# Performance work log

Measured on AMD Instinct MI355X. Metric: run time of the kernel, lower is better.

## Reference

```python
import jax, jax.numpy as jnp
import numpy as np

B, S, D, H = 4, 1024, 1024, 16
DK = D // H
MASK_WEIGHT_0 = 1.0   # weight for key-type 0 (from (weight, mask_mat) tuple)
MASK_WEIGHT_1 = 0.5   # weight for key-type 1
NEG_INF = -1.0e9


def setup_inputs() -> dict:
    key = jax.random.key(0)
    ks = jax.random.split(key, 10)
    wscale = 0.02
    return {
        "query": jax.random.normal(ks[0], (B, S, D), jnp.float32),
        "key_x": jax.random.normal(ks[1], (B, S, D), jnp.float32),
        "value": jax.random.normal(ks[2], (B, S, D), jnp.float32),
        "mask0": jax.random.randint(ks[3], (B, S, S), 0, 2, jnp.int32),
        "mask1": jax.random.randint(ks[4], (B, S, S), 0, 2, jnp.int32),
        "Wq":  wscale * jax.random.normal(ks[5], (D, D), jnp.float32),
        "Wk0": wscale * jax.random.normal(ks[6], (D, D), jnp.float32),
        "Wk1": wscale * jax.random.normal(ks[7], (D, D), jnp.float32),
        "Wv":  wscale * jax.random.normal(ks[8], (D, D), jnp.float32),
        "Wo":  wscale * jax.random.normal(ks[9], (D, D), jnp.float32),
    }


def _heads(x, W):
    # torch nn.Linear: x @ W.T ; then view(B,S,H,DK).transpose(1,2)
    return (x @ W.T).reshape(B, S, H, DK).transpose(0, 2, 1, 3)  # [B,H,S,DK]


def reference(query, key_x, value, mask0, mask1, Wq, Wk0, Wk1, Wv, Wo):
    q = _heads(query, Wq)          # [B,H,S,DK]
    k0 = _heads(key_x, Wk0)
    k1 = _heads(key_x, Wk1)
    v = _heads(value, Wv)
    scale = 1.0 / jnp.sqrt(jnp.float32(DK))

    def masked_score(k, mask, weight):
        s = jnp.einsum('bhqd,bhkd->bhqk', q, k) * scale       # [B,H,S,S]
        keep = (mask != 0)[:, None, :, :]                     # broadcast over heads
        # (score * weight*keep).masked_fill(mask==0, -1e9)
        return jnp.where(keep, s * weight, NEG_INF)

    scores = masked_score(k0, mask0, MASK_WEIGHT_0) + masked_score(k1, mask1, MASK_WEIGHT_1)
    p_attn = jax.nn.sigmoid(scores)                           # activation='sigmoid'
    x = jnp.einsum('bhqk,bhkd->bhqd', p_attn, v)              # [B,H,S,DK]
    x = x.transpose(0, 2, 1, 3).reshape(B, S, D)
    return x @ Wo.T                                            # output_linear (dropout p=0)
```

## Files before the change

### kernel.cpp

```cpp
#include <hip/hip_runtime.h>

#define B_  4
#define S_  1024
#define D_  1024
#define H_  16
#define DK_ 64

typedef __attribute__((ext_vector_type(8)))  short bf16x8;
typedef __attribute__((ext_vector_type(4)))  short bf16x4;
typedef __attribute__((ext_vector_type(4)))  float f32x4;
typedef __attribute__((ext_vector_type(16))) float f32x16;

static __device__ __forceinline__ unsigned short f2bf(float f) {
  union { float f; unsigned u; } v; v.f = f;
  unsigned r = v.u + 0x7FFFu + ((v.u >> 16) & 1u);
  return (unsigned short)(r >> 16);
}

static __device__ __forceinline__ unsigned cvtpk(float lo, float hi) {
  unsigned r;
  asm("v_cvt_pk_bf16_f32 %0, %1, %2" : "=v"(r) : "v"(lo), "v"(hi));
  return r;
}
static __device__ __forceinline__ void plswap(unsigned &a, unsigned &b) {
  asm volatile("v_permlane32_swap_b32 %0, %1" : "+v"(a), "+v"(b));
}

typedef __attribute__((address_space(1))) const void gc_t;
typedef __attribute__((address_space(3))) void lds_t;
static __device__ __forceinline__ void gload_lds16(const void* g, void* l) {
  __builtin_amdgcn_global_load_lds((gc_t*)g, (lds_t*)l, 16, 0, 0);
}

#define TM_ (1u << 22)
#define WM_ (1u << 20)

#define CEXP_ (-0.18033688011112042f)

__global__ __launch_bounds__(256)
void prep(const float* __restrict__ q, const float* __restrict__ k,
          const float* __restrict__ v,
          const float* __restrict__ w0, const float* __restrict__ w1,
          const float* __restrict__ w2, const float* __restrict__ w3,
          const float* __restrict__ w4, unsigned short* __restrict__ out,
          const int* __restrict__ m0, const int* __restrict__ m1,
          unsigned long long* __restrict__ pk)
{
  if (blockIdx.x < 8192) {
    const size_t u = ((size_t)blockIdx.x * 256 + threadIdx.x) * 8;
    unsigned short t[8];
    unsigned short* dst;
    size_t off;
    if (u < (size_t)3 * TM_) {
      int seg = (int)(u >> 22); off = u & (TM_ - 1);
      const float* src = seg == 0 ? q : (seg == 1 ? k : v);
      dst = out + (size_t)seg * TM_ + off;
      float4 f0 = *(const float4*)(src + off);
      float4 f1 = *(const float4*)(src + off + 4);
      t[0]=f2bf(f0.x); t[1]=f2bf(f0.y); t[2]=f2bf(f0.z); t[3]=f2bf(f0.w);
      t[4]=f2bf(f1.x); t[5]=f2bf(f1.y); t[6]=f2bf(f1.z); t[7]=f2bf(f1.w);
    } else {
      size_t uu = u - (size_t)3 * TM_;
      int seg = (int)(uu >> 20); off = uu & (WM_ - 1);
      dst = out + (size_t)3 * TM_ + (size_t)seg * WM_ + off;
      if (seg == 0) {
        float4 f0 = *(const float4*)(w0 + off);
        float4 f1 = *(const float4*)(w0 + off + 4);
        t[0]=f2bf(CEXP_*f0.x); t[1]=f2bf(CEXP_*f0.y);
        t[2]=f2bf(CEXP_*f0.z); t[3]=f2bf(CEXP_*f0.w);
        t[4]=f2bf(CEXP_*f1.x); t[5]=f2bf(CEXP_*f1.y);
        t[6]=f2bf(CEXP_*f1.z); t[7]=f2bf(CEXP_*f1.w);
      } else if (seg == 1) {
        float4 a0 = *(const float4*)(w1 + off);
        float4 a1 = *(const float4*)(w1 + off + 4);
        float4 b0 = *(const float4*)(w2 + off);
        float4 b1 = *(const float4*)(w2 + off + 4);
        t[0]=f2bf(a0.x+0.5f*b0.x); t[1]=f2bf(a0.y+0.5f*b0.y);
        t[2]=f2bf(a0.z+0.5f*b0.z); t[3]=f2bf(a0.w+0.5f*b0.w);
        t[4]=f2bf(a1.x+0.5f*b1.x); t[5]=f2bf(a1.y+0.5f*b1.y);
        t[6]=f2bf(a1.z+0.5f*b1.z); t[7]=f2bf(a1.w+0.5f*b1.w);
      } else {
        const float* src = (seg == 2) ? w3 : w4;
        float4 f0 = *(const float4*)(src + off);
        float4 f1 = *(const float4*)(src + off + 4);
        t[0]=f2bf(f0.x); t[1]=f2bf(f0.y); t[2]=f2bf(f0.z); t[3]=f2bf(f0.w);
        t[4]=f2bf(f1.x); t[5]=f2bf(f1.y); t[6]=f2bf(f1.z); t[7]=f2bf(f1.w);
      }
    }
    *(bf16x8*)dst = *(bf16x8*)t;
  } else {
    const int bidm = blockIdx.x - 8192;
    const int wid  = bidm * 4 + (threadIdx.x >> 6);
    const int lane = threadIdx.x & 63;
    const int word = wid & 15, row = wid >> 4;
    const size_t g = (size_t)row * S_ + word * 64 + lane;
    const bool bit = (m0[g] != 0) & (m1[g] != 0);
    const unsigned long long m = __ballot(bit);
    if (lane == 0) pk[wid] = m;
  }
}

__global__ __launch_bounds__(256, 4)
void proj_gemm(const unsigned short* __restrict__ qbf,
               const unsigned short* __restrict__ kbf,
               const unsigned short* __restrict__ vbf,
               const unsigned short* __restrict__ wbf,
               unsigned short* __restrict__ Qb, unsigned short* __restrict__ Kh,
               unsigned short* __restrict__ Vth)
{
  __shared__ unsigned short As[128][64];
  __shared__ unsigned short Ws[128][64];

  const int tid = threadIdx.x, bid = blockIdx.x;
  const int xcd = bid & 7, c = bid >> 3;
  const int L = xcd * 96 + c;
  const int which = L >> 8;
  const int rem = L & 255;
  const int nt = rem >> 5, mt = rem & 31;
  const int m0 = mt * 128, n0 = nt * 128;
  const int w = tid >> 6, l = tid & 63;
  const int lr = l & 15, lg = l >> 4;
  const int wr = w >> 1, wc = w & 1;

  const unsigned short* A = (which == 0) ? qbf : (which == 1) ? kbf : vbf;
  const unsigned short* W = wbf + (size_t)which * WM_;

  const f32x4 fzero = {0.f, 0.f, 0.f, 0.f};
  f32x4 acc[4][4];
#pragma unroll
  for (int m = 0; m < 4; m++)
#pragma unroll
    for (int n = 0; n < 4; n++) acc[m][n] = fzero;

  const int srow8 = l >> 3;
  const int sg    = ((l & 7) ^ srow8) * 8;
  const int rc0 = ((lg)     ^ (lr & 7)) * 8;
  const int rc1 = ((4 + lg) ^ (lr & 7)) * 8;

  const unsigned short* aBase = A + (size_t)(m0 + w*32 + srow8) * 1024 + sg;
  const unsigned short* wBase = W + (size_t)(n0 + w*32 + srow8) * 1024 + sg;

  for (int kk = 0; kk < 1024; kk += 64) {
#pragma unroll
    for (int cc = 0; cc < 4; ++cc)
      gload_lds16(aBase + (size_t)cc * 8 * 1024 + kk, &As[w*32 + cc*8][0]);
#pragma unroll
    for (int cc = 0; cc < 4; ++cc)
      gload_lds16(wBase + (size_t)cc * 8 * 1024 + kk, &Ws[w*32 + cc*8][0]);
    __syncthreads();

#pragma unroll
    for (int ks = 0; ks < 2; ++ks) {
      const int rc = ks ? rc1 : rc0;
      bf16x8 af[4], bfr[4];
#pragma unroll
      for (int m = 0; m < 4; m++) af[m]  = *(const bf16x8*)&As[wr*64 + m*16 + lr][rc];
#pragma unroll
      for (int n = 0; n < 4; n++) bfr[n] = *(const bf16x8*)&Ws[wc*64 + n*16 + lr][rc];
#pragma unroll
      for (int m = 0; m < 4; m++)
#pragma unroll
        for (int n = 0; n < 4; n++)
          acc[m][n] = __builtin_amdgcn_mfma_f32_16x16x32_bf16(af[m], bfr[n], acc[m][n], 0, 0, 0);
    }
    __syncthreads();
  }

  if (which == 2) {
#pragma unroll
    for (int m = 0; m < 4; m++) {
      const int row = m0 + wr*64 + m*16 + lg*4;
      const int b = row >> 10, s = row & 1023;
#pragma unroll
      for (int n = 0; n < 4; n++) {
        const int col = n0 + wc*64 + n*16 + lr;
        const int h = col >> 6, dk = col & 63;
        unsigned short tv[4] = {f2bf(acc[m][n][0]), f2bf(acc[m][n][1]),
                                f2bf(acc[m][n][2]), f2bf(acc[m][n][3])};
        const size_t a = ((size_t)((b*H_ + h)*DK_ + dk)) * S_
                       + (size_t)(s & ~63) + ((((s >> 3) & 7) ^ (dk & 7)) << 3) + (s & 7);
        *(bf16x4*)(Vth + a) = *(bf16x4*)tv;
      }
    }
  } else if (which == 0) {
#pragma unroll
    for (int m = 0; m < 4; m++) {
      const int row = m0 + wr*64 + m*16 + lg*4;
#pragma unroll
      for (int n = 0; n < 4; n++) {
        const int col = n0 + wc*64 + n*16 + lr;
#pragma unroll
        for (int r = 0; r < 4; r++)
          Qb[(size_t)(row + r) * 1024 + col] = f2bf(acc[m][n][r]);
      }
    }
  } else {
#pragma unroll
    for (int m = 0; m < 4; m++) {
      const int row = m0 + wr*64 + m*16 + lg*4;
#pragma unroll
      for (int n = 0; n < 4; n++) {
        const int col = n0 + wc*64 + n*16 + lr;
        const int h = col >> 6, dk = col & 63;
#pragma unroll
        for (int r = 0; r < 4; r++) {
          const int rr = row + r;
          const int b = rr >> 10, s = rr & 1023;
          const size_t a = ((size_t)((b*H_ + h)*S_ + s)) * 64
                         + (((dk >> 3) ^ (s & 7)) << 3) + (dk & 7);
          Kh[a] = f2bf(acc[m][n][r]);
        }
      }
    }
  }
}

__global__ __launch_bounds__(256, 4)
void out_gemm(const unsigned short* __restrict__ A,
              const unsigned short* __restrict__ W, float* __restrict__ C)
{
  __shared__ unsigned short As[128][64];
  __shared__ unsigned short Ws2[64][64];

  const int tid = threadIdx.x, bid = blockIdx.x;
  const int xcd = bid & 7, idx = bid >> 3;
  const int mt = (xcd << 2) | (idx & 3);
  const int nt = idx >> 2;
  const int m0 = mt * 128, n0 = nt * 64;
  const int w = tid >> 6, l = tid & 63;
  const int lr = l & 15, lg = l >> 4;
  const int wr = w >> 1, wc = w & 1;

  const f32x4 fzero = {0.f, 0.f, 0.f, 0.f};
  f32x4 acc[4][2];
#pragma unroll
  for (int m = 0; m < 4; m++)
#pragma unroll
    for (int n = 0; n < 2; n++) acc[m][n] = fzero;

  const int srow8 = l >> 3;
  const int sg    = ((l & 7) ^ srow8) * 8;
  const int rc0 = ((lg)     ^ (lr & 7)) * 8;
  const int rc1 = ((4 + lg) ^ (lr & 7)) * 8;

  const unsigned short* aBase = A + (size_t)(m0 + w*32 + srow8) * 1024 + sg;
  const unsigned short* wBase = W + (size_t)(n0 + w*16 + srow8) * 1024 + sg;

  for (int kk = 0; kk < 1024; kk += 64) {
#pragma unroll
    for (int cc = 0; cc < 4; ++cc)
      gload_lds16(aBase + (size_t)cc * 8 * 1024 + kk, &As[w*32 + cc*8][0]);
#pragma unroll
    for (int cc = 0; cc < 2; ++cc)
      gload_lds16(wBase + (size_t)cc * 8 * 1024 + kk, &Ws2[w*16 + cc*8][0]);
    __syncthreads();

#pragma unroll
    for (int ks = 0; ks < 2; ++ks) {
      const int rc = ks ? rc1 : rc0;
      bf16x8 af[4], bfr[2];
#pragma unroll
      for (int m = 0; m < 4; m++) af[m]  = *(const bf16x8*)&As[wr*64 + m*16 + lr][rc];
#pragma unroll
      for (int n = 0; n < 2; n++) bfr[n] = *(const bf16x8*)&Ws2[wc*32 + n*16 + lr][rc];
#pragma unroll
      for (int m = 0; m < 4; m++)
#pragma unroll
        for (int n = 0; n < 2; n++)
          acc[m][n] = __builtin_amdgcn_mfma_f32_16x16x32_bf16(af[m], bfr[n], acc[m][n], 0, 0, 0);
    }
    __syncthreads();
  }

#pragma unroll
  for (int m = 0; m < 4; m++) {
    const int row = m0 + wr*64 + m*16 + lg*4;
#pragma unroll
    for (int n = 0; n < 2; n++) {
      const int col = n0 + wc*32 + n*16 + lr;
#pragma unroll
      for (int r = 0; r < 4; r++)
        C[(size_t)(row + r) * 1024 + col] = acc[m][n][r];
    }
  }
}

__global__ __launch_bounds__(512)
void attn_kernel(const unsigned short* __restrict__ Q,
                 const unsigned short* __restrict__ Kh,
                 const unsigned short* __restrict__ Vth,
                 const unsigned long long* __restrict__ mpk,
                 unsigned short* __restrict__ X)
{
  __shared__ unsigned short Ks[2][2][4096];
  __shared__ unsigned short Vs[2][2][4096];

  const int tid  = threadIdx.x;
  const int bid0 = blockIdx.x;
  const int bid = ((bid0 & 7) << 6) | (bid0 >> 3);
  const int qt = bid & 7, h = (bid >> 3) & 15, b = bid >> 7;
  const int q0 = qt * 128;
  const int w8 = tid >> 6, lw = tid & 63;
  const int grp = w8 >> 2, qw = w8 & 3;
  const int l31 = lw & 31, hh = lw >> 5, l7 = lw & 7;
  const int bh = b * H_ + h;

  bf16x8 qf[4];
  {
    const unsigned short* qp = Q + ((size_t)(b*S_ + q0 + qw*32 + l31)) * D_ + h*DK_ + hh*8;
#pragma unroll
    for (int ds = 0; ds < 4; ++ds) qf[ds] = *(const bf16x8*)(qp + ds*16);
  }
  const size_t mbase = ((size_t)(b*S_ + q0 + qw*32 + l31)) * 16 + grp*8;

  f32x16 acc0, acc1;
#pragma unroll
  for (int r = 0; r < 16; ++r) { acc0[r] = 0.f; acc1[r] = 0.f; }

  const unsigned short* gp[4];
  unsigned short* lb[4];
  int stp[4];
#pragma unroll
  for (int c = 0; c < 4; ++c) {
    const int e = qw*4 + c;
    const int bu = e >> 3, s = e & 7;
    lb[c] = (bu == 0 ? &Ks[grp][0][0] : &Vs[grp][0][0]) + s*512;
    if (bu == 0) {
      gp[c]  = Kh + (size_t)bh * 65536 + grp*32768 + s*512 + lw*8;
      stp[c] = 4096;
    } else {
      gp[c]  = Vth + ((size_t)(bh*DK_ + s*8 + (lw >> 3))) * S_ + grp*512 + (lw & 7) * 8;
      stp[c] = 64;
    }
  }

#define STAGE(nxt)                                                     \
  {                                                                    \
    _Pragma("unroll")                                                  \
    for (int c = 0; c < 4; ++c) {                                      \
      gload_lds16(gp[c], lb[c] + (nxt)*4096);                          \
      gp[c] += stp[c];                                                 \
    }                                                                  \
  }

  STAGE(0);
  __syncthreads();
  unsigned long long mw = mpk[mbase];
  int cur = 0;

  for (int t = 0; t < 8; ++t) {
    unsigned long long mw_n = 0;
    if (t < 7) { STAGE(cur ^ 1); mw_n = mpk[mbase + t + 1]; }

#pragma unroll
    for (int sub = 0; sub < 2; ++sub) {
      const int rbase = (sub*32 + l31) * 64;
      f32x16 sv;
#pragma unroll
      for (int r = 0; r < 16; ++r) sv[r] = 0.f;
      __builtin_amdgcn_s_setprio(1);
#pragma unroll
      for (int ds = 0; ds < 4; ++ds) {
        const int g = (((ds*2 + hh) ^ l7)) * 8;
        const bf16x8 kf = *(const bf16x8*)&Ks[grp][cur][rbase + g];
        sv = __builtin_amdgcn_mfma_f32_32x32x16_bf16(kf, qf[ds], sv, 0, 0, 0);
      }
      __builtin_amdgcn_s_setprio(0);

      const unsigned am = (unsigned)(mw >> (sub*32 + 4*hh));
      float p[16];
#pragma unroll
      for (int r = 0; r < 16; ++r) {
        const int cbit = (r & 3) + 8*(r >> 2);
        const float e  = __builtin_amdgcn_exp2f(sv[r]);
        const float pr = __builtin_amdgcn_rcpf(1.0f + e);
        p[r] = ((am >> cbit) & 1u) ? pr : 0.f;
      }

      bf16x8 pa[2];
#pragma unroll
      for (int ks = 0; ks < 2; ++ks) {
        const int a0 = ks*8;
        unsigned u0 = cvtpk(p[a0+0], p[a0+1]);
        unsigned u1 = cvtpk(p[a0+2], p[a0+3]);
        unsigned u2 = cvtpk(p[a0+4], p[a0+5]);
        unsigned u3 = cvtpk(p[a0+6], p[a0+7]);
        plswap(u0, u2);
        plswap(u1, u3);
        union { unsigned u[4]; bf16x8 v; } pu;
        pu.u[0] = u0; pu.u[1] = u1; pu.u[2] = u2; pu.u[3] = u3;
        pa[ks] = pu.v;
      }

      __builtin_amdgcn_s_setprio(1);
#pragma unroll
      for (int ks = 0; ks < 2; ++ks) {
        const int g = ((sub*4 + ks*2 + hh) ^ l7) * 8;
        const bf16x8 vb0 = *(const bf16x8*)&Vs[grp][cur][(l31)      * 64 + g];
        const bf16x8 vb1 = *(const bf16x8*)&Vs[grp][cur][(32 + l31) * 64 + g];
        acc0 = __builtin_amdgcn_mfma_f32_32x32x16_bf16(pa[ks], vb0, acc0, 0, 0, 0);
        acc1 = __builtin_amdgcn_mfma_f32_32x32x16_bf16(pa[ks], vb1, acc1, 0, 0, 0);
      }
      __builtin_amdgcn_s_setprio(0);
    }

    if (t < 7) {
      __syncthreads();
      mw = mw_n;
      cur ^= 1;
    }
  }
#undef STAGE

  __syncthreads();
  float2* cmb = (float2*)&Ks[0][0][0];
  if (grp == 1) {
#pragma unroll
    for (int i = 0; i < 8; ++i)
      cmb[(qw*16 + i)*64 + lw] = make_float2(acc0[2*i], acc0[2*i+1]);
#pragma unroll
    for (int i = 0; i < 8; ++i)
      cmb[(qw*16 + 8 + i)*64 + lw] = make_float2(acc1[2*i], acc1[2*i+1]);
  }
  __syncthreads();
  if (grp == 0) {
#pragma unroll
    for (int i = 0; i < 8; ++i) {
      float2 v = cmb[(qw*16 + i)*64 + lw];
      acc0[2*i] += v.x; acc0[2*i+1] += v.y;
    }
#pragma unroll
    for (int i = 0; i < 8; ++i) {
      float2 v = cmb[(qw*16 + 8 + i)*64 + lw];
      acc1[2*i] += v.x; acc1[2*i+1] += v.y;
    }
#pragma unroll
    for (int r = 0; r < 16; ++r) {
      const int qrow = q0 + qw*32 + (r & 3) + 8*(r >> 2) + 4*hh;
      unsigned short* xp = X + ((size_t)(b*S_ + qrow)) * D_ + h*DK_ + l31;
      xp[0]  = f2bf(acc0[r]);
      xp[32] = f2bf(acc1[r]);
    }
  }
}

extern "C" void kernel_launch(void* const* d_in, const int* in_sizes, int n_in,
                              void* d_out, int out_size, void* d_ws, size_t ws_size,
                              hipStream_t stream)
{
  const float* query = (const float*)d_in[0];
  const float* key_x = (const float*)d_in[1];
  const float* value = (const float*)d_in[2];
  const int*   mask0 = (const int*)d_in[3];
  const int*   mask1 = (const int*)d_in[4];
  const float* Wq    = (const float*)d_in[5];
  const float* Wk0   = (const float*)d_in[6];
  const float* Wk1   = (const float*)d_in[7];
  const float* Wv    = (const float*)d_in[8];
  const float* Wo    = (const float*)d_in[9];

  unsigned short* ws = (unsigned short*)d_ws;
  unsigned short* qbf = ws;
  unsigned short* kbf = ws + (size_t)TM_;
  unsigned short* vbf = ws + (size_t)2 * TM_;
  unsigned short* wbf = ws + (size_t)3 * TM_;
  unsigned short* Qb  = ws + (size_t)3 * TM_ + 4 * WM_;
  unsigned short* Kh  = Qb  + (size_t)TM_;
  unsigned short* Vth = Kh  + (size_t)TM_;
  unsigned long long* mpk = (unsigned long long*)(Vth + (size_t)TM_);
  unsigned short* Xb = qbf;

  prep<<<dim3(8192 + 16384), dim3(256), 0, stream>>>(
      query, key_x, value, Wq, Wk0, Wk1, Wv, Wo, ws, mask0, mask1, mpk);

  proj_gemm<<<dim3(768), dim3(256), 0, stream>>>(qbf, kbf, vbf, wbf,
                                                 Qb, Kh, Vth);

  attn_kernel<<<dim3(B_ * H_ * (S_ / 128)), dim3(512), 0, stream>>>(
      Qb, Kh, Vth, mpk, Xb);

  out_gemm<<<dim3(512), dim3(256), 0, stream>>>(Xb, wbf + (size_t)3 * WM_,
                                                (float*)d_out);
}
```

Baseline: 103.1 us.

## Move mask packing into projection GEMM launch and grid-stride the conversion kernel

The mask bit-packing moves out of the prep kernel and into extra blocks of the projection GEMM launch. Each block now reads int4 vectors and uses four ballots with an interleaved bit layout, and the attention kernel's bit-extraction indexing changes to match. The fp32-to-bf16 conversion becomes a grid-stride kernel with 2048 blocks, and the GEMM tile order is swapped so mt varies slowest. The aim is to overlap the memory-bound mask packing with the compute-bound GEMM and to cut per-thread mask-read overhead, at the cost of a remapped bit layout that must stay consistent across kernels.

Measured after the change: 96.40 us. -6.5%, faster.

```diff
diff --git a/kernel.cpp b/kernel.cpp
--- a/kernel.cpp
+++ b/kernel.cpp
@@ -38,39 +38,30 @@
 #define CEXP_ (-0.18033688011112042f)
 
 __global__ __launch_bounds__(256)
-void prep(const float* __restrict__ q, const float* __restrict__ k,
-          const float* __restrict__ v,
-          const float* __restrict__ w0, const float* __restrict__ w1,
-          const float* __restrict__ w2, const float* __restrict__ w3,
-          const float* __restrict__ w4, unsigned short* __restrict__ out,
-          const int* __restrict__ m0, const int* __restrict__ m1,
-          unsigned long long* __restrict__ pk)
+void cvt_ws(const float* __restrict__ q, const float* __restrict__ k,
+            const float* __restrict__ v,
+            const float* __restrict__ w0, const float* __restrict__ w1,
+            const float* __restrict__ w2, const float* __restrict__ w3,
+            const float* __restrict__ w4, unsigned short* __restrict__ out)
 {
-  if (blockIdx.x < 8192) {
-    const size_t u = ((size_t)blockIdx.x * 256 + threadIdx.x) * 8;
+  const size_t total = (size_t)3 * TM_ + 4 * WM_;
+  const size_t step  = (size_t)2048 * 256 * 8;
+  for (size_t u = ((size_t)blockIdx.x * 256 + threadIdx.x) * 8; u < total;
+       u += step) {
     unsigned short t[8];
-    unsigned short* dst;
-    size_t off;
     if (u < (size_t)3 * TM_) {
-      int seg = (int)(u >> 22); off = u & (TM_ - 1);
+      const int seg = (int)(u >> 22);
+      const size_t off = u & (TM_ - 1);
       const float* src = seg == 0 ? q : (seg == 1 ? k : v);
-      dst = out + (size_t)seg * TM_ + off;
       float4 f0 = *(const float4*)(src + off);
       float4 f1 = *(const float4*)(src + off + 4);
       t[0]=f2bf(f0.x); t[1]=f2bf(f0.y); t[2]=f2bf(f0.z); t[3]=f2bf(f0.w);
       t[4]=f2bf(f1.x); t[5]=f2bf(f1.y); t[6]=f2bf(f1.z); t[7]=f2bf(f1.w);
     } else {
-      size_t uu = u - (size_t)3 * TM_;
-      int seg = (int)(uu >> 20); off = uu & (WM_ - 1);
-      dst = out + (size_t)3 * TM_ + (size_t)seg * WM_ + off;
-      if (seg == 0) {
-        float4 f0 = *(const float4*)(w0 + off);
-        float4 f1 = *(const float4*)(w0 + off + 4);
-        t[0]=f2bf(CEXP_*f0.x); t[1]=f2bf(CEXP_*f0.y);
-        t[2]=f2bf(CEXP_*f0.z); t[3]=f2bf(CEXP_*f0.w);
-        t[4]=f2bf(CEXP_*f1.x); t[5]=f2bf(CEXP_*f1.y);
-        t[6]=f2bf(CEXP_*f1.z); t[7]=f2bf(CEXP_*f1.w);
-      } else if (seg == 1) {
+      const size_t uu = u - (size_t)3 * TM_;
+      const int seg = (int)(uu >> 20);
+      const size_t off = uu & (WM_ - 1);
+      if (seg == 1) {
         float4 a0 = *(const float4*)(w1 + off);
         float4 a1 = *(const float4*)(w1 + off + 4);
         float4 b0 = *(const float4*)(w2 + off);
@@ -80,23 +71,17 @@
         t[4]=f2bf(a1.x+0.5f*b1.x); t[5]=f2bf(a1.y+0.5f*b1.y);
         t[6]=f2bf(a1.z+0.5f*b1.z); t[7]=f2bf(a1.w+0.5f*b1.w);
       } else {
-        const float* src = (seg == 2) ? w3 : w4;
+        const float sc = (seg == 0) ? CEXP_ : 1.0f;
+        const float* src = (seg == 0) ? w0 : (seg == 2 ? w3 : w4);
         float4 f0 = *(const float4*)(src + off);
         float4 f1 = *(const float4*)(src + off + 4);
-        t[0]=f2bf(f0.x); t[1]=f2bf(f0.y); t[2]=f2bf(f0.z); t[3]=f2bf(f0.w);
-        t[4]=f2bf(f1.x); t[5]=f2bf(f1.y); t[6]=f2bf(f1.z); t[7]=f2bf(f1.w);
-      }
-    }
-    *(bf16x8*)dst = *(bf16x8*)t;
-  } else {
-    const int bidm = blockIdx.x - 8192;
-    const int wid  = bidm * 4 + (threadIdx.x >> 6);
-    const int lane = threadIdx.x & 63;
-    const int word = wid & 15, row = wid >> 4;
-    const size_t g = (size_t)row * S_ + word * 64 + lane;
-    const bool bit = (m0[g] != 0) & (m1[g] != 0);
-    const unsigned long long m = __ballot(bit);
-    if (lane == 0) pk[wid] = m;
+        t[0]=f2bf(sc*f0.x); t[1]=f2bf(sc*f0.y);
+        t[2]=f2bf(sc*f0.z); t[3]=f2bf(sc*f0.w);
+        t[4]=f2bf(sc*f1.x); t[5]=f2bf(sc*f1.y);
+        t[6]=f2bf(sc*f1.z); t[7]=f2bf(sc*f1.w);
+      }
+    }
+    *(bf16x8*)(out + u) = *(bf16x8*)t;
   }
 }
 
@@ -106,17 +91,40 @@
                const unsigned short* __restrict__ vbf,
                const unsigned short* __restrict__ wbf,
                unsigned short* __restrict__ Qb, unsigned short* __restrict__ Kh,
-               unsigned short* __restrict__ Vth)
+               unsigned short* __restrict__ Vth,
+               const int* __restrict__ ma, const int* __restrict__ mb,
+               unsigned long long* __restrict__ pk)
 {
   __shared__ unsigned short As[128][64];
   __shared__ unsigned short Ws[128][64];
 
   const int tid = threadIdx.x, bid = blockIdx.x;
+
+  if (bid >= 768) {
+    const int row = bid - 768;
+    const int w4  = tid >> 6, lw = tid & 63;
+    const int4 a  = *(const int4*)(ma + (size_t)row*1024 + w4*256 + lw*4);
+    const int4 b  = *(const int4*)(mb + (size_t)row*1024 + w4*256 + lw*4);
+    const unsigned long long b0 = __ballot((a.x != 0) & (b.x != 0));
+    const unsigned long long b1 = __ballot((a.y != 0) & (b.y != 0));
+    const unsigned long long b2 = __ballot((a.z != 0) & (b.z != 0));
+    const unsigned long long b3 = __ballot((a.w != 0) & (b.w != 0));
+    if (lw < 4) {
+      const unsigned long long wv =
+            ((b0 >> (16*lw)) & 0xFFFFull)
+         | (((b1 >> (16*lw)) & 0xFFFFull) << 16)
+         | (((b2 >> (16*lw)) & 0xFFFFull) << 32)
+         | (((b3 >> (16*lw)) & 0xFFFFull) << 48);
+      pk[(size_t)row*16 + w4*4 + lw] = wv;
+    }
+    return;
+  }
+
   const int xcd = bid & 7, c = bid >> 3;
   const int L = xcd * 96 + c;
   const int which = L >> 8;
   const int rem = L & 255;
-  const int nt = rem >> 5, mt = rem & 31;
+  const int mt = rem >> 3, nt = rem & 7;
   const int m0 = mt * 128, n0 = nt * 128;
   const int w = tid >> 6, l = tid & 63;
   const int lr = l & 15, lg = l >> 4;
@@ -367,14 +375,14 @@
       }
       __builtin_amdgcn_s_setprio(0);
 
-      const unsigned am = (unsigned)(mw >> (sub*32 + 4*hh));
+      const unsigned long long ams = mw >> (8*sub + hh);
       float p[16];
 #pragma unroll
       for (int r = 0; r < 16; ++r) {
-        const int cbit = (r & 3) + 8*(r >> 2);
+        const int cbit = 16*(r & 3) + 2*(r >> 2);
         const float e  = __builtin_amdgcn_exp2f(sv[r]);
         const float pr = __builtin_amdgcn_rcpf(1.0f + e);
-        p[r] = ((am >> cbit) & 1u) ? pr : 0.f;
+        p[r] = ((ams >> cbit) & 1ull) ? pr : 0.f;
       }
 
       bf16x8 pa[2];
@@ -470,11 +478,11 @@
   unsigned long long* mpk = (unsigned long long*)(Vth + (size_t)TM_);
   unsigned short* Xb = qbf;
 
-  prep<<<dim3(8192 + 16384), dim3(256), 0, stream>>>(
-      query, key_x, value, Wq, Wk0, Wk1, Wv, Wo, ws, mask0, mask1, mpk);
-
-  proj_gemm<<<dim3(768), dim3(256), 0, stream>>>(qbf, kbf, vbf, wbf,
-                                                 Qb, Kh, Vth);
+  cvt_ws<<<dim3(2048), dim3(256), 0, stream>>>(
+      query, key_x, value, Wq, Wk0, Wk1, Wv, Wo, ws);
+
+  proj_gemm<<<dim3(768 + 4096), dim3(256), 0, stream>>>(
+      qbf, kbf, vbf, wbf, Qb, Kh, Vth, mask0, mask1, mpk);
 
   attn_kernel<<<dim3(B_ * H_ * (S_ / 128)), dim3(512), 0, stream>>>(
       Qb, Kh, Vth, mpk, Xb);
```
